# Kernel tuning notes

Measured on AMD Instinct MI355X. Metric: run time of the kernel, lower is better.

## Reference

```python
import jax, jax.numpy as jnp
import numpy as np

B, S, H, E, C, V = 512, 256, 768, 6, 10, 3


def setup_inputs() -> dict:
    key = jax.random.key(0)
    ks = jax.random.split(key, 16)

    def w(k, shape):
        fan_in = shape[-1]
        return jax.random.normal(k, shape, dtype=jnp.float32) / np.sqrt(fan_in)

    return {
        'x': jax.random.randint(ks[0], (B, S), 0, V, dtype=jnp.int64),
        'emb': w(ks[1], (V, E)),
        'W_fx': w(ks[2], (H, E)), 'W_fh': w(ks[3], (H, H)), 'b_f': w(ks[4], (H, 1)),
        'W_ix': w(ks[5], (H, E)), 'W_ih': w(ks[6], (H, H)), 'b_i': w(ks[7], (H, 1)),
        'W_ox': w(ks[8], (H, E)), 'W_oh': w(ks[9], (H, H)), 'b_o': w(ks[10], (H, 1)),
        'W_cx': w(ks[11], (H, E)), 'b_c': w(ks[12], (H, 1)),
        'W_ph': w(ks[13], (C, H)), 'b_p': w(ks[14], (C, 1)),
        'c_init': jax.random.normal(ks[15], (H, B), dtype=jnp.float32) / np.sqrt(B),
    }


def reference(x, emb, W_fx, W_fh, b_f, W_ix, W_ih, b_i, W_ox, W_oh, b_o,
              W_cx, b_c, W_ph, b_p, c_init):
    # Embed tokens: [B, S] -> [B, S, E] -> time-major [S, E, B]
    xe = jnp.transpose(emb[x], (1, 2, 0))
    xs = xe[: S - 1]  # loop runs seq_length - 1 steps

    def step(carry, x_t):
        c_prev, _ = carry  # c_prev: [H, B], x_t: [E, B]
        f_t = jax.nn.sigmoid(W_fx @ x_t + W_fh @ c_prev + b_f)
        i_t = jax.nn.sigmoid(W_ix @ x_t + W_ih @ c_prev + b_i)
        o_t = jax.nn.sigmoid(W_ox @ x_t + W_oh @ c_prev + b_o)
        c_t = jax.nn.sigmoid(W_cx @ x_t + b_c) * i_t + c_prev * f_t
        h_t = jnp.tanh(c_t) * o_t
        return (c_t, h_t), None

    h0 = jnp.zeros((H, B), dtype=c_init.dtype)
    (c_fin, h_fin), _ = jax.lax.scan(step, (c_init, h0), xs)
    p_t = W_ph @ h_fin + b_p  # [C, B]
    return jax.nn.log_softmax(p_t.T, axis=-1)  # [B, C]
```

## Files before the change

### kernel.cpp

```cpp
#include <hip/hip_runtime.h>


typedef _Float16 f16x8 __attribute__((ext_vector_type(8)));
typedef _Float16 f16x4 __attribute__((ext_vector_type(4)));
typedef float    f32x4 __attribute__((ext_vector_type(4)));

#define Hdim  768
#define Bdim  512
#define Sdim  256
#define NSTEP 255
#define Edim  6
#define NCls  10
#define NGRP  16
#define NRB   12
#define GC    32
#define HB    64
#define NKK   24
#define CSTR  776
#define XSTR  260
#define PLANE (Bdim * Hdim)
#define SCL      4096.0f
#define SCL_INV  2.44140625e-4f

#define WP_FRAGS   (2 * NRB * 4 * NKK * 64)
#define WS_CBUF    0u
#define WS_HFIN    (2u * 2u * PLANE * 2u)
#define WS_BAR     (WS_HFIN + Bdim * Hdim * 4u)
#define WS_WPK     (WS_BAR + 4096u)
#define WS_BAR_BYTES (NGRP * 16u * 4u)

__device__ __forceinline__ float sigf(float z) { return 1.0f / (1.0f + __expf(-z)); }

__device__ __forceinline__ f32x4 mf(f16x8 a, f16x8 b, f32x4 c) {
    return __builtin_amdgcn_mfma_f32_16x16x32_f16(a, b, c, 0, 0, 0);
}

__global__ void __launch_bounds__(256)
prep_w(const float* __restrict__ Wfh, const float* __restrict__ Wih,
       _Float16* __restrict__ wpk)
{
    const int fid  = blockIdx.x * 256 + threadIdx.x;
    const int lane = fid & 63;
    const int t1   = fid >> 6;
    const int kk   = t1 % NKK;
    const int gi   = t1 / NKK;
    const int sub  = gi & 3;
    const int t3   = gi >> 2;
    const int rb   = t3 % NRB;
    const int gate = t3 / NRB;
    const int q = lane >> 4, r = lane & 15;
    const int row = rb * 64 + sub * 16 + r;
    const int col = kk * 32 + q * 8;
    const float* src = (gate ? Wih : Wfh) + (size_t)row * Hdim + col;
    f16x8 hi, lo;
    #pragma unroll
    for (int j = 0; j < 8; ++j) {
        const float v = src[j];
        const _Float16 h = (_Float16)v;
        hi[j] = h;
        lo[j] = (_Float16)((v - (float)h) * SCL);
    }
    *(f16x8*)&wpk[(size_t)fid * 8] = hi;
    *(f16x8*)&wpk[((size_t)WP_FRAGS + fid) * 8] = lo;
}

__global__ void __launch_bounds__(512, 2)
lstm_persist(const int* __restrict__ xk, const float* __restrict__ emb,
             const float* __restrict__ Wfx, const float* __restrict__ bfv,
             const float* __restrict__ Wix, const float* __restrict__ biv,
             const float* __restrict__ Wox, const float* __restrict__ Woh,
             const float* __restrict__ bov,
             const float* __restrict__ Wcx, const float* __restrict__ bcv,
             const float* __restrict__ cinit,
             const _Float16* __restrict__ wpk,
             _Float16* __restrict__ cbuf, float* __restrict__ hfin,
             unsigned int* __restrict__ bar)
{
    __shared__ __align__(16) _Float16 ldsH[GC * CSTR];
    __shared__ __align__(16) _Float16 ldsM[GC * CSTR];
    __shared__ __align__(16) float    tbl[3 * HB * 4];
    __shared__ __align__(16) float    zbuf[HB * GC];
    __shared__ __align__(4)  unsigned char xtok[GC * XSTR];
    __shared__ int s_flag;

    const int tid  = threadIdx.x;
    const int w    = tid >> 6;
    const int lane = tid & 63;
    const int q    = lane >> 4;
    const int r    = lane & 15;
    const int gt   = w >> 2;
    const int sub  = w & 3;
    const int bid  = blockIdx.x;
    const int g    = bid & 15;
    const int rb   = bid >> 4;
    const int blkh0 = rb * HB;
    const int gc0   = g * GC;
    const int hq0   = blkh0 + sub * 16 + q * 4;
    const int gi    = (gt * NRB + rb) * 4 + sub;

    if (tid == 0) s_flag = 0;
    __syncthreads();
    if (tid < 256) {
        if (xk[(size_t)gc0 * Sdim + 2 * tid + 1] != 0) s_flag = 1;
    }
    if (tid < 3 * HB) {
        const int v  = tid >> 6;
        const int hl = tid & 63;
        const int hg = blkh0 + hl;
        float pf = bfv[hg], pi = biv[hg], po = bov[hg], pc = bcv[hg];
        #pragma unroll
        for (int e = 0; e < Edim; ++e) {
            const float ev = emb[v * Edim + e];
            pf += Wfx[hg * Edim + e] * ev;
            pi += Wix[hg * Edim + e] * ev;
            po += Wox[hg * Edim + e] * ev;
            pc += Wcx[hg * Edim + e] * ev;
        }
        float* t = &tbl[(v * HB + hl) * 4];
        t[0] = pf; t[1] = pi; t[2] = po; t[3] = sigf(pc);
    }
    __syncthreads();
    const int is64 = (s_flag == 0);

    {
        const int col   = tid >> 4;
        const int sbase = (tid & 15) * 16;
        const size_t rowb = (size_t)(gc0 + col) * Sdim;
        for (int k2 = 0; k2 < 16; ++k2) {
            const int s0 = sbase + k2;
            const size_t idx = rowb + s0;
            xtok[col * XSTR + s0] = (unsigned char)xk[is64 ? (idx << 1) : idx];
        }
    }

    f16x8 whi[NKK];
    #pragma unroll
    for (int kk = 0; kk < NKK; ++kk)
        whi[kk] = *(const f16x8*)&wpk[((size_t)(gi * NKK + kk) * 64 + lane) * 8];
    const _Float16* wloB = wpk + ((size_t)WP_FRAGS + (size_t)(gi * NKK) * 64 + lane) * 8;

    float cst[2][4];
    #pragma unroll
    for (int ct = 0; ct < 2; ++ct) {
        const int b = gc0 + ct * 16 + r;
        #pragma unroll
        for (int reg = 0; reg < 4; ++reg)
            cst[ct][reg] = cinit[(size_t)(hq0 + reg) * Bdim + b];
    }

    for (int i = 0; i < 48; ++i) {
        const int idx = tid + i * 512;
        const int col = idx & 31, k = idx >> 5;
        const float v = cinit[(size_t)k * Bdim + gc0 + col];
        const _Float16 h = (_Float16)v;
        ldsH[col * CSTR + k] = h;
        ldsM[col * CSTR + k] = (_Float16)((v - (float)h) * SCL);
    }

    for (int s = 0; s < NSTEP; ++s) {
        __syncthreads();

        f32x4 a0h = {0,0,0,0}, a0x = {0,0,0,0}, a1h = {0,0,0,0}, a1x = {0,0,0,0};
        #pragma unroll
        for (int kk = 0; kk < NKK; ++kk) {
            const f16x8 wl = *(const f16x8*)&wloB[(size_t)kk * 64 * 8];
            const int lo = kk * 32 + q * 8;
            const f16x8 bh0 = *(const f16x8*)&ldsH[ r       * CSTR + lo];
            const f16x8 bm0 = *(const f16x8*)&ldsM[ r       * CSTR + lo];
            const f16x8 bh1 = *(const f16x8*)&ldsH[(16 + r) * CSTR + lo];
            const f16x8 bm1 = *(const f16x8*)&ldsM[(16 + r) * CSTR + lo];
            a0h = mf(whi[kk], bh0, a0h);
            a0x = mf(whi[kk], bm0, a0x);
            a0x = mf(wl,      bh0, a0x);
            a1h = mf(whi[kk], bh1, a1h);
            a1x = mf(whi[kk], bm1, a1x);
            a1x = mf(wl,      bh1, a1x);
        }
        if (gt) {
            #pragma unroll
            for (int ct = 0; ct < 2; ++ct) {
                const f32x4 zh = ct ? a1h : a0h;
                const f32x4 zx = ct ? a1x : a0x;
                #pragma unroll
                for (int reg = 0; reg < 4; ++reg)
                    zbuf[(sub * 16 + q * 4 + reg) * GC + ct * 16 + r] =
                        zh[reg] + zx[reg] * SCL_INV;
            }
        }
        __syncthreads();

        if (!gt) {
            if (s != NSTEP - 1) {
                _Float16* cwH = cbuf + (size_t)(((s + 1) & 1) * 2) * PLANE;
                _Float16* cwM = cwH + PLANE;
                #pragma unroll
                for (int ct = 0; ct < 2; ++ct) {
                    const int bl = ct * 16 + r;
                    const int v  = xtok[bl * XSTR + s];
                    const float* tb = &tbl[(v * HB + sub * 16 + q * 4) * 4];
                    const f32x4 zh = ct ? a1h : a0h;
                    const f32x4 zx = ct ? a1x : a0x;
                    f16x4 cvh, cvm;
                    #pragma unroll
                    for (int reg = 0; reg < 4; ++reg) {
                        const float zf = zh[reg] + zx[reg] * SCL_INV;
                        const float zi = zbuf[(sub * 16 + q * 4 + reg) * GC + bl];
                        const float* tt = tb + reg * 4;
                        const float fg = sigf(zf + tt[0]);
                        const float ig = sigf(zi + tt[1]);
                        const float cn = tt[3] * ig + cst[ct][reg] * fg;
                        cst[ct][reg] = cn;
                        const _Float16 ch = (_Float16)cn;
                        cvh[reg] = ch;
                        cvm[reg] = (_Float16)((cn - (float)ch) * SCL);
                    }
                    unsigned long long uh, um;
                    __builtin_memcpy(&uh, &cvh, 8);
                    __builtin_memcpy(&um, &cvm, 8);
                    const size_t eo = (size_t)(gc0 + bl) * Hdim + hq0;
                    __hip_atomic_store((unsigned long long*)&cwH[eo], uh,
                                       __ATOMIC_RELAXED, __HIP_MEMORY_SCOPE_AGENT);
                    __hip_atomic_store((unsigned long long*)&cwM[eo], um,
                                       __ATOMIC_RELAXED, __HIP_MEMORY_SCOPE_AGENT);
                }
            } else {
                f32x4 o0h = {0,0,0,0}, o0x = {0,0,0,0}, o1h = {0,0,0,0}, o1x = {0,0,0,0};
                const int arow = blkh0 + sub * 16 + r;
                #pragma unroll
                for (int kk = 0; kk < NKK; ++kk) {
                    const float* wp = Woh + (size_t)arow * Hdim + kk * 32 + q * 8;
                    f16x8 who;
                    #pragma unroll
                    for (int j = 0; j < 8; ++j) who[j] = (_Float16)wp[j];
                    const int lo = kk * 32 + q * 8;
                    const f16x8 bh0 = *(const f16x8*)&ldsH[ r       * CSTR + lo];
                    const f16x8 bm0 = *(const f16x8*)&ldsM[ r       * CSTR + lo];
                    const f16x8 bh1 = *(const f16x8*)&ldsH[(16 + r) * CSTR + lo];
                    const f16x8 bm1 = *(const f16x8*)&ldsM[(16 + r) * CSTR + lo];
                    o0h = mf(who, bh0, o0h);  o0x = mf(who, bm0, o0x);
                    o1h = mf(who, bh1, o1h);  o1x = mf(who, bm1, o1x);
                }
                #pragma unroll
                for (int ct = 0; ct < 2; ++ct) {
                    const int bl = ct * 16 + r;
                    const int v  = xtok[bl * XSTR + s];
                    const float* tb = &tbl[(v * HB + sub * 16 + q * 4) * 4];
                    const f32x4 zh = ct ? a1h : a0h;
                    const f32x4 zx = ct ? a1x : a0x;
                    const f32x4 zoh = ct ? o1h : o0h;
                    const f32x4 zox = ct ? o1x : o0x;
                    f32x4 hv;
                    #pragma unroll
                    for (int reg = 0; reg < 4; ++reg) {
                        const float zf = zh[reg] + zx[reg] * SCL_INV;
                        const float zi = zbuf[(sub * 16 + q * 4 + reg) * GC + bl];
                        const float zo = zoh[reg] + zox[reg] * SCL_INV;
                        const float* tt = tb + reg * 4;
                        const float fg = sigf(zf + tt[0]);
                        const float ig = sigf(zi + tt[1]);
                        const float og = sigf(zo + tt[2]);
                        const float cn = tt[3] * ig + cst[ct][reg] * fg;
                        const float e  = __expf(-2.0f * fabsf(cn));
                        const float th = __builtin_copysignf((1.0f - e) / (1.0f + e), cn);
                        hv[reg] = th * og;
                    }
                    *(f32x4*)&hfin[(size_t)(gc0 + bl) * Hdim + hq0] = hv;
                }
            }
        }

        if (s < NSTEP - 1) {
            asm volatile("s_waitcnt vmcnt(0)" ::: "memory");
            __syncthreads();
            if (w == 0) {
                if (lane == 0)
                    __hip_atomic_store(&bar[g * 16 + rb], (unsigned)(s + 1),
                                       __ATOMIC_RELAXED, __HIP_MEMORY_SCOPE_AGENT);
                const unsigned tgt = (unsigned)(s + 1);
                while (true) {
                    unsigned vv = tgt;
                    if (lane < NRB)
                        vv = __hip_atomic_load(&bar[g * 16 + lane],
                                               __ATOMIC_RELAXED, __HIP_MEMORY_SCOPE_AGENT);
                    if (__all(vv >= tgt)) break;
                    __builtin_amdgcn_s_sleep(2);
                }
            }
            __syncthreads();
            const _Float16* crH = cbuf + (size_t)(((s + 1) & 1) * 2) * PLANE;
            const _Float16* crM = crH + PLANE;
            const int col = tid >> 4, j = tid & 15;
            const size_t rowo = (size_t)(gc0 + col) * Hdim;
            unsigned long long th[12], tm[12];
            #pragma unroll
            for (int i = 0; i < 12; ++i)
                th[i] = __hip_atomic_load((unsigned long long*)&crH[rowo + (j + 16 * i) * 4],
                                          __ATOMIC_RELAXED, __HIP_MEMORY_SCOPE_AGENT);
            #pragma unroll
            for (int i = 0; i < 12; ++i)
                tm[i] = __hip_atomic_load((unsigned long long*)&crM[rowo + (j + 16 * i) * 4],
                                          __ATOMIC_RELAXED, __HIP_MEMORY_SCOPE_AGENT);
            #pragma unroll
            for (int i = 0; i < 12; ++i) {
                *(unsigned long long*)&ldsH[col * CSTR + (j + 16 * i) * 4] = th[i];
                *(unsigned long long*)&ldsM[col * CSTR + (j + 16 * i) * 4] = tm[i];
            }
        }
    }
}

__global__ void __launch_bounds__(64)
proj_kernel(const float* __restrict__ hfin, const float* __restrict__ Wph,
            const float* __restrict__ bpv, float* __restrict__ out)
{
    const int b = blockIdx.x;
    const int lane = threadIdx.x;
    float acc[NCls];
    #pragma unroll
    for (int c = 0; c < NCls; ++c) acc[c] = 0.f;
    const float* hb = &hfin[(size_t)b * Hdim];
    for (int i = 0; i < Hdim / 64; ++i) {
        const float hv = hb[lane + i * 64];
        #pragma unroll
        for (int c = 0; c < NCls; ++c)
            acc[c] += Wph[c * Hdim + lane + i * 64] * hv;
    }
    #pragma unroll
    for (int c = 0; c < NCls; ++c) {
        float v = acc[c];
        #pragma unroll
        for (int off = 32; off > 0; off >>= 1)
            v += __shfl_xor(v, off, 64);
        acc[c] = v + bpv[c];
    }
    float m = acc[0];
    #pragma unroll
    for (int c = 1; c < NCls; ++c) m = fmaxf(m, acc[c]);
    float ssum = 0.f;
    #pragma unroll
    for (int c = 0; c < NCls; ++c) ssum += __expf(acc[c] - m);
    const float lse = m + __logf(ssum);
    if (lane < NCls) out[b * NCls + lane] = acc[lane] - lse;
}

extern "C" void kernel_launch(void* const* d_in, const int* in_sizes, int n_in,
                              void* d_out, int out_size, void* d_ws, size_t ws_size,
                              hipStream_t stream)
{
    const int*   xk    = (const int*)d_in[0];
    const float* emb   = (const float*)d_in[1];
    const float* Wfx   = (const float*)d_in[2];
    const float* Wfh   = (const float*)d_in[3];
    const float* bfv   = (const float*)d_in[4];
    const float* Wix   = (const float*)d_in[5];
    const float* Wih   = (const float*)d_in[6];
    const float* biv   = (const float*)d_in[7];
    const float* Wox   = (const float*)d_in[8];
    const float* Woh   = (const float*)d_in[9];
    const float* bov   = (const float*)d_in[10];
    const float* Wcx   = (const float*)d_in[11];
    const float* bcv   = (const float*)d_in[12];
    const float* Wph   = (const float*)d_in[13];
    const float* bpv   = (const float*)d_in[14];
    const float* cinit = (const float*)d_in[15];

    char* ws = (char*)d_ws;
    _Float16*     cbuf = (_Float16*)(ws + WS_CBUF);
    float*        hfin = (float*)(ws + WS_HFIN);
    unsigned int* bar  = (unsigned int*)(ws + WS_BAR);
    _Float16*     wpk  = (_Float16*)(ws + WS_WPK);

    hipMemsetAsync(bar, 0, WS_BAR_BYTES, stream);

    prep_w<<<dim3(WP_FRAGS / 256), dim3(256), 0, stream>>>(Wfh, Wih, wpk);

    lstm_persist<<<dim3(NGRP * NRB), dim3(512), 0, stream>>>(
        xk, emb, Wfx, bfv, Wix, biv, Wox, Woh, bov, Wcx, bcv,
        cinit, wpk, cbuf, hfin, bar);

    proj_kernel<<<dim3(Bdim), dim3(64), 0, stream>>>(hfin, Wph, bpv, (float*)d_out);
}
```

Baseline: 2.196 ms.

## Keep low weight halves in registers and replace block barrier with per-wave flag signaling

The low-precision weight fragments are now preloaded into registers alongside the high halves, so they are no longer fetched from global memory every step; launch bounds drop to one block per SM to make room for the extra registers. The cross-block step barrier is restructured: the four cell-update waves bump a shared-memory counter and the last one publishes the block's step flag, and every wave then spins on the flags itself instead of doing two __syncthreads around a single-wave poll. The state reload is split into two phases to cut live registers. This trades lower occupancy and heavier polling traffic for less global weight traffic and shorter barrier latency, and it relies on the existing top-of-loop sync for LDS ordering.

```diff
diff --git a/kernel.cpp b/kernel.cpp
--- a/kernel.cpp
+++ b/kernel.cpp
@@ -64,7 +64,7 @@
     *(f16x8*)&wpk[((size_t)WP_FRAGS + fid) * 8] = lo;
 }
 
-__global__ void __launch_bounds__(512, 2)
+__global__ void __launch_bounds__(512, 1)
 lstm_persist(const int* __restrict__ xk, const float* __restrict__ emb,
              const float* __restrict__ Wfx, const float* __restrict__ bfv,
              const float* __restrict__ Wix, const float* __restrict__ biv,
@@ -82,6 +82,7 @@
     __shared__ __align__(16) float    zbuf[HB * GC];
     __shared__ __align__(4)  unsigned char xtok[GC * XSTR];
     __shared__ int s_flag;
+    __shared__ unsigned int fdone;
 
     const int tid  = threadIdx.x;
     const int w    = tid >> 6;
@@ -98,7 +99,7 @@
     const int hq0   = blkh0 + sub * 16 + q * 4;
     const int gi    = (gt * NRB + rb) * 4 + sub;
 
-    if (tid == 0) s_flag = 0;
+    if (tid == 0) { s_flag = 0; fdone = 0u; }
     __syncthreads();
     if (tid < 256) {
         if (xk[(size_t)gc0 * Sdim + 2 * tid + 1] != 0) s_flag = 1;
@@ -133,11 +134,12 @@
         }
     }
 
-    f16x8 whi[NKK];
-    #pragma unroll
-    for (int kk = 0; kk < NKK; ++kk)
+    f16x8 whi[NKK], wlo[NKK];
+    #pragma unroll
+    for (int kk = 0; kk < NKK; ++kk) {
         whi[kk] = *(const f16x8*)&wpk[((size_t)(gi * NKK + kk) * 64 + lane) * 8];
-    const _Float16* wloB = wpk + ((size_t)WP_FRAGS + (size_t)(gi * NKK) * 64 + lane) * 8;
+        wlo[kk] = *(const f16x8*)&wpk[((size_t)WP_FRAGS + (size_t)(gi * NKK + kk) * 64 + lane) * 8];
+    }
 
     float cst[2][4];
     #pragma unroll
@@ -163,7 +165,6 @@
         f32x4 a0h = {0,0,0,0}, a0x = {0,0,0,0}, a1h = {0,0,0,0}, a1x = {0,0,0,0};
         #pragma unroll
         for (int kk = 0; kk < NKK; ++kk) {
-            const f16x8 wl = *(const f16x8*)&wloB[(size_t)kk * 64 * 8];
             const int lo = kk * 32 + q * 8;
             const f16x8 bh0 = *(const f16x8*)&ldsH[ r       * CSTR + lo];
             const f16x8 bm0 = *(const f16x8*)&ldsM[ r       * CSTR + lo];
@@ -171,10 +172,10 @@
             const f16x8 bm1 = *(const f16x8*)&ldsM[(16 + r) * CSTR + lo];
             a0h = mf(whi[kk], bh0, a0h);
             a0x = mf(whi[kk], bm0, a0x);
-            a0x = mf(wl,      bh0, a0x);
+            a0x = mf(wlo[kk], bh0, a0x);
             a1h = mf(whi[kk], bh1, a1h);
             a1x = mf(whi[kk], bm1, a1x);
-            a1x = mf(wl,      bh1, a1x);
+            a1x = mf(wlo[kk], bh1, a1x);
         }
         if (gt) {
             #pragma unroll
@@ -223,6 +224,14 @@
                     __hip_atomic_store((unsigned long long*)&cwM[eo], um,
                                        __ATOMIC_RELAXED, __HIP_MEMORY_SCOPE_AGENT);
                 }
+                asm volatile("s_waitcnt vmcnt(0)" ::: "memory");
+                if (lane == 0) {
+                    const unsigned old = __hip_atomic_fetch_add(&fdone, 1u,
+                                         __ATOMIC_ACQ_REL, __HIP_MEMORY_SCOPE_WORKGROUP);
+                    if (old == 4u * (unsigned)s + 3u)
+                        __hip_atomic_store(&bar[g * 16 + rb], (unsigned)(s + 1),
+                                           __ATOMIC_RELAXED, __HIP_MEMORY_SCOPE_AGENT);
+                }
             } else {
                 f32x4 o0h = {0,0,0,0}, o0x = {0,0,0,0}, o1h = {0,0,0,0}, o1x = {0,0,0,0};
                 const int arow = blkh0 + sub * 16 + r;
@@ -270,40 +279,38 @@
         }
 
         if (s < NSTEP - 1) {
-            asm volatile("s_waitcnt vmcnt(0)" ::: "memory");
-            __syncthreads();
-            if (w == 0) {
-                if (lane == 0)
-                    __hip_atomic_store(&bar[g * 16 + rb], (unsigned)(s + 1),
-                                       __ATOMIC_RELAXED, __HIP_MEMORY_SCOPE_AGENT);
-                const unsigned tgt = (unsigned)(s + 1);
-                while (true) {
-                    unsigned vv = tgt;
-                    if (lane < NRB)
-                        vv = __hip_atomic_load(&bar[g * 16 + lane],
-                                               __ATOMIC_RELAXED, __HIP_MEMORY_SCOPE_AGENT);
-                    if (__all(vv >= tgt)) break;
-                    __builtin_amdgcn_s_sleep(2);
-                }
-            }
-            __syncthreads();
+            const unsigned tgt = (unsigned)(s + 1);
+            while (true) {
+                unsigned vv = tgt;
+                if (lane < NRB)
+                    vv = __hip_atomic_load(&bar[g * 16 + lane],
+                                           __ATOMIC_RELAXED, __HIP_MEMORY_SCOPE_AGENT);
+                if (__all(vv >= tgt)) break;
+                __builtin_amdgcn_s_sleep(1);
+            }
             const _Float16* crH = cbuf + (size_t)(((s + 1) & 1) * 2) * PLANE;
             const _Float16* crM = crH + PLANE;
             const int col = tid >> 4, j = tid & 15;
             const size_t rowo = (size_t)(gc0 + col) * Hdim;
-            unsigned long long th[12], tm[12];
-            #pragma unroll
-            for (int i = 0; i < 12; ++i)
-                th[i] = __hip_atomic_load((unsigned long long*)&crH[rowo + (j + 16 * i) * 4],
-                                          __ATOMIC_RELAXED, __HIP_MEMORY_SCOPE_AGENT);
-            #pragma unroll
-            for (int i = 0; i < 12; ++i)
-                tm[i] = __hip_atomic_load((unsigned long long*)&crM[rowo + (j + 16 * i) * 4],
-                                          __ATOMIC_RELAXED, __HIP_MEMORY_SCOPE_AGENT);
-            #pragma unroll
-            for (int i = 0; i < 12; ++i) {
-                *(unsigned long long*)&ldsH[col * CSTR + (j + 16 * i) * 4] = th[i];
-                *(unsigned long long*)&ldsM[col * CSTR + (j + 16 * i) * 4] = tm[i];
+            {
+                unsigned long long th[12];
+                #pragma unroll
+                for (int i = 0; i < 12; ++i)
+                    th[i] = __hip_atomic_load((unsigned long long*)&crH[rowo + (j + 16 * i) * 4],
+                                              __ATOMIC_RELAXED, __HIP_MEMORY_SCOPE_AGENT);
+                #pragma unroll
+                for (int i = 0; i < 12; ++i)
+                    *(unsigned long long*)&ldsH[col * CSTR + (j + 16 * i) * 4] = th[i];
+            }
+            {
+                unsigned long long tm[12];
+                #pragma unroll
+                for (int i = 0; i < 12; ++i)
+                    tm[i] = __hip_atomic_load((unsigned long long*)&crM[rowo + (j + 16 * i) * 4],
+                                              __ATOMIC_RELAXED, __HIP_MEMORY_SCOPE_AGENT);
+                #pragma unroll
+                for (int i = 0; i < 12; ++i)
+                    *(unsigned long long*)&ldsM[col * CSTR + (j + 16 * i) * 4] = tm[i];
             }
         }
     }
```

Measured after the change: 2.582 ms. 17.6% more time.
